# Kernel tuning notes

Hardware: AMD Instinct MI355X
Metric: run time of the kernel (lower is better)

Reference implementation:

```python
import jax, jax.numpy as jnp
import numpy as np

DIM = 1536
NH = 12
HD = DIM // NH  # 128
F_, H_, W_ = 16, 16, 16
L = F_ * H_ * W_  # 4096


def _precompute_freqs(dim, max_positions, base=10000.0):
    # [max_positions, dim//2] angles
    half = dim // 2
    inv = 1.0 / base ** (np.arange(0, half * 2, 2, dtype=np.float32) / (half * 2))
    pos = np.arange(max_positions, dtype=np.float32)
    return pos[:, None] * inv[None, :]


def _get_3d_freqs(head_dim, F, H, W, base=10000.0):
    half_hd = head_dim // 2
    n_t = max(1, head_dim // 4 // 2)
    n_h = max(1, head_dim * 3 // 8 // 2)
    n_w = half_hd - n_t - n_h
    ft = _precompute_freqs(n_t * 2, F, base)  # [F, n_t]
    fh = _precompute_freqs(n_h * 2, H, base)  # [H, n_h]
    fw = _precompute_freqs(n_w * 2, W, base)  # [W, n_w]
    f_idx = np.broadcast_to(ft[:, None, None, :], (F, H, W, n_t))
    h_idx = np.broadcast_to(fh[None, :, None, :], (F, H, W, n_h))
    w_idx = np.broadcast_to(fw[None, None, :, :], (F, H, W, n_w))
    return np.concatenate([f_idx, h_idx, w_idx], axis=-1).reshape(F * H * W, half_hd)


def setup_inputs() -> dict:
    key = jax.random.key(0)
    ks = jax.random.split(key, 9)
    s = 1.0 / np.sqrt(DIM)
    x = jax.random.normal(ks[0], (1, L, DIM), dtype=jnp.float32)
    freqs = jnp.asarray(_get_3d_freqs(HD, F_, H_, W_), dtype=jnp.float32)
    Wq = jax.random.normal(ks[1], (DIM, DIM), dtype=jnp.float32) * s
    bq = jax.random.normal(ks[2], (DIM,), dtype=jnp.float32) * 0.01
    Wk = jax.random.normal(ks[3], (DIM, DIM), dtype=jnp.float32) * s
    bk = jax.random.normal(ks[4], (DIM,), dtype=jnp.float32) * 0.01
    Wv = jax.random.normal(ks[5], (DIM, DIM), dtype=jnp.float32) * s
    bv = jax.random.normal(ks[6], (DIM,), dtype=jnp.float32) * 0.01
    Wo = jax.random.normal(ks[7], (DIM, DIM), dtype=jnp.float32) * s
    bo = jax.random.normal(ks[8], (DIM,), dtype=jnp.float32) * 0.01
    return {"x": x, "freqs": freqs, "Wq": Wq, "bq": bq, "Wk": Wk, "bk": bk,
            "Wv": Wv, "bv": bv, "Wo": Wo, "bo": bo}


def _apply_rotary(t, cos_v, sin_v):
    # t: [B, Nh, L, Hd]; cos_v/sin_v: [L, Hd//2]
    B, Nh, Lq, Hd = t.shape
    t2 = t.reshape(B, Nh, Lq, Hd // 2, 2)
    x0, x1 = t2[..., 0], t2[..., 1]
    r0 = x0 * cos_v - x1 * sin_v
    r1 = x0 * sin_v + x1 * cos_v
    return jnp.stack([r0, r1], axis=-1).reshape(B, Nh, Lq, Hd)


def reference(x, freqs, Wq, bq, Wk, bk, Wv, bv, Wo, bo):
    B, Lq, D = x.shape
    Nh, Hd = NH, D // NH
    q = (x @ Wq + bq).reshape(B, Lq, Nh, Hd).transpose(0, 2, 1, 3)
    k = (x @ Wk + bk).reshape(B, Lq, Nh, Hd).transpose(0, 2, 1, 3)
    v = (x @ Wv + bv).reshape(B, Lq, Nh, Hd).transpose(0, 2, 1, 3)
    cos_v = jnp.cos(freqs)  # [L, Hd//2]
    sin_v = jnp.sin(freqs)
    q = _apply_rotary(q, cos_v, sin_v)
    k = _apply_rotary(k, cos_v, sin_v)
    scale = 1.0 / jnp.sqrt(jnp.asarray(Hd, dtype=x.dtype))
    scores = jnp.einsum('bhqd,bhkd->bhqk', q, k) * scale
    attn = jax.nn.softmax(scores, axis=-1)
    out = jnp.einsum('bhqk,bhkd->bhqd', attn, v)
    out = out.transpose(0, 2, 1, 3).reshape(B, Lq, D)
    return out @ Wo + bo
```

## Files before the change

### kernel.cpp

```cpp
#include <hip/hip_runtime.h>

#define DIM 1536
#define NH  12
#define HD  128
#define SEQ 4096

typedef unsigned short u16;
typedef unsigned int   u32;
typedef __attribute__((ext_vector_type(8))) short bf16x8;
typedef __attribute__((ext_vector_type(4))) float f32x4;
typedef __attribute__((ext_vector_type(16))) float f32x16;

static __device__ __forceinline__ u16 f2bf(float f) {
    u32 u = __float_as_uint(f);
    u32 r = u + 0x7FFFu + ((u >> 16) & 1u);
    return (u16)(r >> 16);
}
static __device__ __forceinline__ float bf2f(u16 h) {
    return __uint_as_float(((u32)h) << 16);
}
static __device__ __forceinline__ u32 pack2(float a, float b) {
    return (u32)f2bf(a) | ((u32)f2bf(b) << 16);
}

#define GLL(g, s) __builtin_amdgcn_global_load_lds( \
    (const __attribute__((address_space(1))) void*)(g), \
    (__attribute__((address_space(3))) void*)(s), 16, 0, 0)

__global__ __launch_bounds__(256) void k_cvt_x(const float* __restrict__ x, u16* __restrict__ xb) {
    int gid = blockIdx.x * 256 + threadIdx.x;
    const float4* p = (const float4*)x + (size_t)gid * 2;
    float4 a = p[0], b = p[1];
    uint4 o;
    o.x = pack2(a.x, a.y); o.y = pack2(a.z, a.w);
    o.z = pack2(b.x, b.y); o.w = pack2(b.z, b.w);
    *(uint4*)(xb + (size_t)gid * 8) = o;
}

__global__ __launch_bounds__(256) void k_transpose_w(const float* __restrict__ Wq, const float* __restrict__ Wk,
                                                     const float* __restrict__ Wv, const float* __restrict__ Wo,
                                                     u16* __restrict__ wqkv, u16* __restrict__ wot) {
    __shared__ float tile[32][33];
    int z = blockIdx.z;
    const float* W = z == 0 ? Wq : z == 1 ? Wk : z == 2 ? Wv : Wo;
    u16* out = z < 3 ? (wqkv + (size_t)z * DIM * DIM) : wot;
    int tx = threadIdx.x, ty = threadIdx.y;
    int c0 = blockIdx.x * 32, r0 = blockIdx.y * 32;
#pragma unroll
    for (int i = 0; i < 4; i++)
        tile[ty + i * 8][tx] = W[(size_t)(r0 + ty + i * 8) * DIM + c0 + tx];
    __syncthreads();
#pragma unroll
    for (int i = 0; i < 4; i++)
        out[(size_t)(c0 + ty + i * 8) * DIM + r0 + tx] = f2bf(tile[tx][ty + i * 8]);
}

__global__ __launch_bounds__(256) void k_tr_v(const u16* __restrict__ vb, u16* __restrict__ vt) {
    __shared__ u16 tile[32][33];
    int h = blockIdx.z;
    int l0 = blockIdx.x * 32, d0 = blockIdx.y * 32;
    int tx = threadIdx.x, ty = threadIdx.y;
    const u16* src = vb + (size_t)h * SEQ * HD;
    u16* dst = vt + (size_t)h * HD * SEQ;
#pragma unroll
    for (int i = 0; i < 4; i++)
        tile[ty + i * 8][tx] = src[(size_t)(l0 + ty + i * 8) * HD + d0 + tx];
    __syncthreads();
#pragma unroll
    for (int i = 0; i < 4; i++)
        dst[(size_t)(d0 + ty + i * 8) * SEQ + l0 + tx] = tile[tx][ty + i * 8];
}

__global__ __launch_bounds__(256) void k_prep(const float* __restrict__ fr, const float* __restrict__ bq,
                                              const float* __restrict__ bk, const float* __restrict__ bv,
                                              float2* __restrict__ cs, float* __restrict__ bqkv) {
    int gid = blockIdx.x * 256 + threadIdx.x;
    float f = fr[gid];
    cs[gid] = make_float2(cosf(f), sinf(f));
    if (gid < 3 * DIM)
        bqkv[gid] = gid < DIM ? bq[gid] : gid < 2 * DIM ? bk[gid - DIM] : bv[gid - 2 * DIM];
}

__global__ __launch_bounds__(256) void k_gemm(const u16* __restrict__ A, const u16* __restrict__ B,
                                              const float* __restrict__ bias, int Kdim, int mode,
                                              u16* __restrict__ qo, u16* __restrict__ ko,
                                              u16* __restrict__ vo, float* __restrict__ outf) {
    __shared__ u16 As[2][128 * 32];
    __shared__ u16 Bs[2][128 * 32];
    const int tid = threadIdx.x;
    const int w = tid >> 6, l = tid & 63;
    const int wr = w >> 1, wc = w & 1;
    const int lr = l & 15, lg = l >> 4;
    int nwg = gridDim.x * gridDim.y;
    int bid = blockIdx.y * gridDim.x + blockIdx.x;
    int swz = (bid & 7) * (nwg >> 3) + (bid >> 3);
    const int m0 = (swz / gridDim.x) * 128, n0 = (swz % gridDim.x) * 128;
    f32x4 acc[4][4] = {};

    const int srow = l >> 2;
    const int scol = (((l & 3) * 16) ^ (((l >> 2) & 3) << 4)) >> 1;

    const int nk = Kdim >> 5;
#pragma unroll
    for (int c2 = 0; c2 < 2; ++c2) {
        int c = w * 2 + c2;
        int row = c * 16 + srow;
        GLL(A + (size_t)(m0 + row) * Kdim + scol, As[0] + c * 512);
        GLL(B + (size_t)(n0 + row) * Kdim + scol, Bs[0] + c * 512);
    }
    __syncthreads();

    int cur = 0;
    for (int t = 0; t < nk; ++t) {
        if (t + 1 < nk) {
            int kt = (t + 1) << 5;
#pragma unroll
            for (int c2 = 0; c2 < 2; ++c2) {
                int c = w * 2 + c2;
                int row = c * 16 + srow;
                GLL(A + (size_t)(m0 + row) * Kdim + kt + scol, As[cur ^ 1] + c * 512);
                GLL(B + (size_t)(n0 + row) * Kdim + kt + scol, Bs[cur ^ 1] + c * 512);
            }
        }
        const u16* Ac = As[cur];
        const u16* Bc = Bs[cur];
        bf16x8 af[4], bg[4];
#pragma unroll
        for (int i = 0; i < 4; i++) {
            int co = (lg * 8) ^ ((lr & 3) << 3);
            af[i] = *(const bf16x8*)(Ac + (wr * 64 + i * 16 + lr) * 32 + co);
            bg[i] = *(const bf16x8*)(Bc + (wc * 64 + i * 16 + lr) * 32 + co);
        }
#pragma unroll
        for (int i = 0; i < 4; i++)
#pragma unroll
            for (int j = 0; j < 4; j++)
                acc[i][j] = __builtin_amdgcn_mfma_f32_16x16x32_bf16(af[i], bg[j], acc[i][j], 0, 0, 0);
        __syncthreads();
        cur ^= 1;
    }

#pragma unroll
    for (int j = 0; j < 4; j++) {
        int gc = n0 + wc * 64 + j * 16 + lr;
        float bb = bias[gc];
#pragma unroll
        for (int i = 0; i < 4; i++) {
            int gr0 = m0 + wr * 64 + i * 16 + lg * 4;
            if (mode == 0) {
                int t = gc / DIM;
                int rr = gc % DIM;
                int hh = rr >> 7, hd = rr & 127;
                u16* dst = t == 0 ? qo : t == 1 ? ko : vo;
                size_t base = (size_t)hh * SEQ * HD + hd;
#pragma unroll
                for (int r = 0; r < 4; r++)
                    dst[base + (size_t)(gr0 + r) * HD] = f2bf(acc[i][j][r] + bb);
            } else {
#pragma unroll
                for (int r = 0; r < 4; r++)
                    outf[(size_t)(gr0 + r) * DIM + gc] = acc[i][j][r] + bb;
            }
        }
    }
}

__global__ __launch_bounds__(256) void k_rope(u16* __restrict__ qb, u16* __restrict__ kb,
                                              const float2* __restrict__ cs) {
    int gid = blockIdx.x * 256 + threadIdx.x;
    const int T = NH * SEQ * 8;
    u16* buf = gid < T ? qb : kb;
    int r = gid < T ? gid : gid - T;
    int hh = r / (SEQ * 8);
    int rr = r % (SEQ * 8);
    int ll = rr >> 3, i0 = (rr & 7) * 8;
    size_t off = ((size_t)hh * SEQ + ll) * HD + 2 * i0;
    uint4 pa = *(const uint4*)(buf + off);
    uint4 pb = *(const uint4*)(buf + off + 8);
    const float4* cp = (const float4*)(cs + (size_t)ll * 64 + i0);
    float4 c0 = cp[0], c1 = cp[1], c2 = cp[2], c3 = cp[3];
    auto rot = [](u32 pk, float cv, float sv) -> u32 {
        float x0 = bf2f((u16)(pk & 0xFFFFu)), x1 = bf2f((u16)(pk >> 16));
        return pack2(x0 * cv - x1 * sv, x0 * sv + x1 * cv);
    };
    uint4 oa, ob;
    oa.x = rot(pa.x, c0.x, c0.y); oa.y = rot(pa.y, c0.z, c0.w);
    oa.z = rot(pa.z, c1.x, c1.y); oa.w = rot(pa.w, c1.z, c1.w);
    ob.x = rot(pb.x, c2.x, c2.y); ob.y = rot(pb.y, c2.z, c2.w);
    ob.z = rot(pb.z, c3.x, c3.y); ob.w = rot(pb.w, c3.z, c3.w);
    *(uint4*)(buf + off) = oa;
    *(uint4*)(buf + off + 8) = ob;
}

__global__ __launch_bounds__(256, 3) void k_attn(const u16* __restrict__ qb, const u16* __restrict__ kbuf,
                                                 const u16* __restrict__ vt, u16* __restrict__ attnb) {
    __shared__ u16 Ks[64 * 128];
    __shared__ u16 Vs[128 * 64];
    __shared__ float MB[128][18];
    const int tid = threadIdx.x;
    const int w = tid >> 6, l = tid & 63;
    const int qh = w & 1, kh = w >> 1;
    const int g = l >> 5, qlane = l & 31;
    const int lr = l & 15, lg = l >> 4;
    int bid = blockIdx.x;
    int gw = (bid & 7) * 96 + (bid >> 3);
    const int h = gw >> 6;
    const int q0 = (gw & 63) << 6;
    const size_t hb = (size_t)h * SEQ * HD;
    constexpr float SCL2 = 0.08838834764831845f * 1.4426950408889634f;
    constexpr float THR = 5.0f;

    const int vrow8 = l >> 3;
    const int vc0 = (((l & 7) * 16) ^ (vrow8 << 4)) >> 1;

    bf16x8 qf[8];
    {
        const u16* qp = qb + hb + (size_t)(q0 + qh * 32 + qlane) * HD + g * 8;
#pragma unroll
        for (int s = 0; s < 8; s++)
            qf[s] = *(const bf16x8*)(qp + s * 16);
    }
    f32x16 O[4] = {};
    float m_run = -1e30f, lsum = 0.f;

    const int krow = kh * 32 + qlane;
    const int ksw = (krow & 7) << 4;
    const int vswl = (qlane & 7) << 4;

    for (int kt = 0; kt < SEQ; kt += 64) {
        __syncthreads();
#pragma unroll
        for (int c = 0; c < 4; c++) {
            int cc = w * 4 + c;
            int key = cc * 4 + lg;
            int kd0 = ((lr * 16) ^ ((key & 7) << 4)) >> 1;
            GLL(kbuf + hb + (size_t)(kt + key) * HD + kd0, Ks + cc * 512);
            int dd = cc * 8 + vrow8;
            GLL(vt + hb + (size_t)dd * SEQ + kt + vc0, Vs + cc * 512);
        }
        __syncthreads();

        f32x16 ST = {};
        const u16* Kp = Ks + krow * 128;
#pragma unroll
        for (int s = 0; s < 8; s++) {
            bf16x8 kf = *(const bf16x8*)(Kp + (((s * 32 + g * 16) ^ ksw) >> 1));
            ST = __builtin_amdgcn_mfma_f32_32x32x16_bf16(kf, qf[s], ST, 0, 0, 0);
        }

        float mx = ST[0];
#pragma unroll
        for (int r = 1; r < 16; r++) mx = fmaxf(mx, ST[r]);
        mx = fmaxf(mx, __shfl_xor(mx, 32));
        float mt = mx * SCL2;
        bool grow = mt > m_run + THR;
        float m_new = grow ? mt : m_run;
        if (__any(grow)) {
            float alpha = grow ? __builtin_amdgcn_exp2f(m_run - m_new) : 1.0f;
            lsum *= alpha;
            m_run = m_new;
#pragma unroll
            for (int db = 0; db < 4; db++)
#pragma unroll
                for (int r = 0; r < 16; r++) O[db][r] *= alpha;
        }
        float ps = 0.f;
#pragma unroll
        for (int r = 0; r < 16; r++) {
            float p = __builtin_amdgcn_exp2f(fmaf(ST[r], SCL2, -m_new));
            ST[r] = p; ps += p;
        }
        lsum += ps;

        u32 pw[2][4];
#pragma unroll
        for (int s2 = 0; s2 < 2; s2++) {
            int rb = s2 * 8;
            u32 a, b2, c2, d2;
            asm("v_cvt_pk_bf16_f32 %0, %1, %2" : "=v"(a)  : "v"(ST[rb + 0]), "v"(ST[rb + 1]));
            asm("v_cvt_pk_bf16_f32 %0, %1, %2" : "=v"(b2) : "v"(ST[rb + 2]), "v"(ST[rb + 3]));
            asm("v_cvt_pk_bf16_f32 %0, %1, %2" : "=v"(c2) : "v"(ST[rb + 4]), "v"(ST[rb + 5]));
            asm("v_cvt_pk_bf16_f32 %0, %1, %2" : "=v"(d2) : "v"(ST[rb + 6]), "v"(ST[rb + 7]));
            asm("v_permlane32_swap_b32 %0, %1" : "+v"(a), "+v"(c2));
            asm("v_permlane32_swap_b32 %0, %1" : "+v"(b2), "+v"(d2));
            pw[s2][0] = a; pw[s2][1] = b2; pw[s2][2] = c2; pw[s2][3] = d2;
        }

#pragma unroll
        for (int s2 = 0; s2 < 2; s2++) {
            union { u32 u[4]; bf16x8 v; } pf;
            pf.u[0] = pw[s2][0]; pf.u[1] = pw[s2][1]; pf.u[2] = pw[s2][2]; pf.u[3] = pw[s2][3];
            int kb2 = kh * 64 + s2 * 32 + g * 16;
#pragma unroll
            for (int db = 0; db < 4; db++) {
                int d = db * 32 + qlane;
                bf16x8 vf = *(const bf16x8*)(Vs + d * 64 + ((kb2 ^ vswl) >> 1));
                O[db] = __builtin_amdgcn_mfma_f32_32x32x16_bf16(vf, pf.v, O[db], 0, 0, 0);
            }
        }
    }

    lsum += __shfl_xor(lsum, 32);

    const int row = qh * 64 + l;
    u16* op = attnb + (size_t)(q0 + qh * 32 + qlane) * DIM + h * HD;
    __syncthreads();
    if (kh == 1) { MB[row][16] = m_run; MB[row][17] = lsum; }
    __syncthreads();
    float a0 = 0.f, a1 = 0.f;
    if (kh == 0) {
        float m1 = MB[row][16], l1 = MB[row][17];
        float mM = fmaxf(m_run, m1);
        a0 = __builtin_amdgcn_exp2f(m_run - mM);
        a1 = __builtin_amdgcn_exp2f(m1 - mM);
        float linv = 1.0f / (lsum * a0 + l1 * a1);
        a0 *= linv; a1 *= linv;
    }
#pragma unroll
    for (int db = 0; db < 4; db++) {
        __syncthreads();
        if (kh == 1) {
#pragma unroll
            for (int r = 0; r < 16; r++) MB[row][r] = O[db][r];
        }
        __syncthreads();
        if (kh == 0) {
#pragma unroll
            for (int r = 0; r < 16; r++) {
                int d = db * 32 + (r & 3) + 8 * (r >> 2) + 4 * g;
                op[d] = f2bf(O[db][r] * a0 + MB[row][r] * a1);
            }
        }
    }
}

extern "C" void kernel_launch(void* const* d_in, const int* in_sizes, int n_in,
                              void* d_out, int out_size, void* d_ws, size_t ws_size,
                              hipStream_t stream) {
    (void)in_sizes; (void)n_in; (void)out_size; (void)ws_size;
    const float* x  = (const float*)d_in[0];
    const float* fr = (const float*)d_in[1];
    const float* Wq = (const float*)d_in[2];
    const float* bq = (const float*)d_in[3];
    const float* Wk = (const float*)d_in[4];
    const float* bk = (const float*)d_in[5];
    const float* Wv = (const float*)d_in[6];
    const float* bv = (const float*)d_in[7];
    const float* Wo = (const float*)d_in[8];
    const float* bo = (const float*)d_in[9];
    float* out = (float*)d_out;

    char* ws = (char*)d_ws;
    size_t off = 0;
    auto alloc = [&](size_t b) { char* p = ws + off; off = (off + b + 255) & ~(size_t)255; return p; };
    u16*   xb    = (u16*)alloc((size_t)SEQ * DIM * 2);
    u16*   wqkv  = (u16*)alloc((size_t)3 * DIM * DIM * 2);
    u16*   wot   = (u16*)alloc((size_t)DIM * DIM * 2);
    float* bqkv  = (float*)alloc((size_t)3 * DIM * 4);
    u16*   qb    = (u16*)alloc((size_t)SEQ * DIM * 2);
    u16*   kb    = (u16*)alloc((size_t)SEQ * DIM * 2);
    u16*   vb    = (u16*)alloc((size_t)SEQ * DIM * 2);
    u16*   vtb   = (u16*)alloc((size_t)SEQ * DIM * 2);
    u16*   attnb = (u16*)alloc((size_t)SEQ * DIM * 2);
    float2* cs   = (float2*)alloc((size_t)SEQ * 64 * 8);

    k_cvt_x<<<3072, 256, 0, stream>>>(x, xb);
    k_transpose_w<<<dim3(48, 48, 4), dim3(32, 8), 0, stream>>>(Wq, Wk, Wv, Wo, wqkv, wot);
    k_prep<<<1024, 256, 0, stream>>>(fr, bq, bk, bv, cs, bqkv);
    k_gemm<<<dim3(36, 32), 256, 0, stream>>>(xb, wqkv, bqkv, DIM, 0, qb, kb, vb, nullptr);
    k_rope<<<3072, 256, 0, stream>>>(qb, kb, cs);
    k_tr_v<<<dim3(128, 4, 12), dim3(32, 8), 0, stream>>>(vb, vtb);
    k_attn<<<768, 256, 0, stream>>>(qb, kb, vtb, attnb);
    k_gemm<<<dim3(12, 32), 256, 0, stream>>>(attnb, wot, bo, DIM, 1, nullptr, nullptr, nullptr, out);
}
```

Before: 283.8 us.

## Triple-buffer GEMM LDS loads with vmcnt waits; raise MFMA priority in attention

The GEMM kernel moves from double to triple-buffered LDS staging. It prefetches two K-tiles ahead and replaces the full __syncthreads with explicit s_waitcnt vmcnt counts plus raw s_barrier, so global-to-LDS loads overlap more with MFMA work. The attention kernel wraps its QK and PV MFMA blocks in s_setprio(1)/s_setprio(0) so the scheduler favours matrix issue across waves. LDS use in the GEMM grows by half, which may reduce occupancy, and the hand-counted vmcnt values must match the number of outstanding loads exactly.

```diff
diff --git a/kernel.cpp b/kernel.cpp
--- a/kernel.cpp
+++ b/kernel.cpp
@@ -85,8 +85,8 @@
                                               const float* __restrict__ bias, int Kdim, int mode,
                                               u16* __restrict__ qo, u16* __restrict__ ko,
                                               u16* __restrict__ vo, float* __restrict__ outf) {
-    __shared__ u16 As[2][128 * 32];
-    __shared__ u16 Bs[2][128 * 32];
+    __shared__ u16 As[3][128 * 32];
+    __shared__ u16 Bs[3][128 * 32];
     const int tid = threadIdx.x;
     const int w = tid >> 6, l = tid & 63;
     const int wr = w >> 1, wc = w & 1;
@@ -99,31 +99,42 @@
 
     const int srow = l >> 2;
     const int scol = (((l & 3) * 16) ^ (((l >> 2) & 3) << 4)) >> 1;
+    const int crow0 = (w * 2) * 16 + srow;
+    const int crow1 = crow0 + 16;
+    const size_t Abase0 = (size_t)(m0 + crow0) * Kdim + scol;
+    const size_t Abase1 = (size_t)(m0 + crow1) * Kdim + scol;
+    const size_t Bbase0 = (size_t)(n0 + crow0) * Kdim + scol;
+    const size_t Bbase1 = (size_t)(n0 + crow1) * Kdim + scol;
+    const int cofs0 = (w * 2) * 512;
+    const int cofs1 = cofs0 + 512;
+
+#define STAGE(buf, kt) do { \
+        GLL(A + Abase0 + (kt), As[buf] + cofs0); \
+        GLL(B + Bbase0 + (kt), Bs[buf] + cofs0); \
+        GLL(A + Abase1 + (kt), As[buf] + cofs1); \
+        GLL(B + Bbase1 + (kt), Bs[buf] + cofs1); \
+    } while (0)
 
     const int nk = Kdim >> 5;
-#pragma unroll
-    for (int c2 = 0; c2 < 2; ++c2) {
-        int c = w * 2 + c2;
-        int row = c * 16 + srow;
-        GLL(A + (size_t)(m0 + row) * Kdim + scol, As[0] + c * 512);
-        GLL(B + (size_t)(n0 + row) * Kdim + scol, Bs[0] + c * 512);
-    }
-    __syncthreads();
-
-    int cur = 0;
+    STAGE(0, 0);
+    STAGE(1, 32);
+
+    int b0 = 0, b1 = 1, b2 = 2;
     for (int t = 0; t < nk; ++t) {
-        if (t + 1 < nk) {
-            int kt = (t + 1) << 5;
-#pragma unroll
-            for (int c2 = 0; c2 < 2; ++c2) {
-                int c = w * 2 + c2;
-                int row = c * 16 + srow;
-                GLL(A + (size_t)(m0 + row) * Kdim + kt + scol, As[cur ^ 1] + c * 512);
-                GLL(B + (size_t)(n0 + row) * Kdim + kt + scol, Bs[cur ^ 1] + c * 512);
-            }
-        }
-        const u16* Ac = As[cur];
-        const u16* Bc = Bs[cur];
+        if (t + 2 < nk) {
+            STAGE(b2, (t + 2) << 5);
+            asm volatile("s_waitcnt vmcnt(8)" ::: "memory");
+        } else if (t + 1 < nk) {
+            asm volatile("s_waitcnt vmcnt(4)" ::: "memory");
+        } else {
+            asm volatile("s_waitcnt vmcnt(0)" ::: "memory");
+        }
+        __builtin_amdgcn_sched_barrier(0);
+        __builtin_amdgcn_s_barrier();
+        asm volatile("" ::: "memory");
+
+        const u16* Ac = As[b0];
+        const u16* Bc = Bs[b0];
         bf16x8 af[4], bg[4];
 #pragma unroll
         for (int i = 0; i < 4; i++) {
@@ -136,9 +147,13 @@
 #pragma unroll
             for (int j = 0; j < 4; j++)
                 acc[i][j] = __builtin_amdgcn_mfma_f32_16x16x32_bf16(af[i], bg[j], acc[i][j], 0, 0, 0);
-        __syncthreads();
-        cur ^= 1;
-    }
+
+        asm volatile("" ::: "memory");
+        __builtin_amdgcn_s_barrier();
+        asm volatile("" ::: "memory");
+        int tmp = b0; b0 = b1; b1 = b2; b2 = tmp;
+    }
+#undef STAGE
 
 #pragma unroll
     for (int j = 0; j < 4; j++) {
@@ -242,11 +257,13 @@
 
         f32x16 ST = {};
         const u16* Kp = Ks + krow * 128;
+        __builtin_amdgcn_s_setprio(1);
 #pragma unroll
         for (int s = 0; s < 8; s++) {
             bf16x8 kf = *(const bf16x8*)(Kp + (((s * 32 + g * 16) ^ ksw) >> 1));
             ST = __builtin_amdgcn_mfma_f32_32x32x16_bf16(kf, qf[s], ST, 0, 0, 0);
         }
+        __builtin_amdgcn_s_setprio(0);
 
         float mx = ST[0];
 #pragma unroll
@@ -286,6 +303,7 @@
             pw[s2][0] = a; pw[s2][1] = b2; pw[s2][2] = c2; pw[s2][3] = d2;
         }
 
+        __builtin_amdgcn_s_setprio(1);
 #pragma unroll
         for (int s2 = 0; s2 < 2; s2++) {
             union { u32 u[4]; bf16x8 v; } pf;
@@ -298,6 +316,7 @@
                 O[db] = __builtin_amdgcn_mfma_f32_32x32x16_bf16(vf, pf.v, O[db], 0, 0, 0);
             }
         }
+        __builtin_amdgcn_s_setprio(0);
     }
 
     lsum += __shfl_xor(lsum, 32);
```

After: 290.7 us. 1.02x slower.
